# Optimization experiments

Measured on AMD Instinct MI355X. Metric: run time of the kernel, lower is better.

The kernel has to match this reference:

```python
import jax, jax.numpy as jnp
from jax import lax
import numpy as np

P, L, T, DEG, D = 100000, 20000, 8, 48, 64  # n_paths, n_links, max_path_len, max_link_degree, state dim
ITERS = 4


def _relu(x):
    return jnp.maximum(x, 0.0)


def _gru_cell(x, h, wih, whh, bih, bhh):
    # PyTorch GRU gate math
    gi = x @ wih.T + bih
    gh = h @ whh.T + bhh
    ir, iz, inn = jnp.split(gi, 3, axis=-1)
    hr, hz, hn = jnp.split(gh, 3, axis=-1)
    r = jax.nn.sigmoid(ir + hr)
    z = jax.nn.sigmoid(iz + hz)
    n = jnp.tanh(inn + r * hn)
    return (1.0 - z) * n + z * h


def _forward(traffic, capacity, link_to_path, path_to_link,
             pe_w1, pe_b1, pe_w2, pe_b2,
             le_w1, le_b1, le_w2, le_b2,
             gru_wih, gru_whh, gru_bih, gru_bhh,
             cell_wih, cell_whh, cell_bih, cell_bhh,
             am_w1, am_b1, am_w2, am_b2, am_w3, am_b3):
    path_state = _relu(_relu(traffic @ pe_w1.T + pe_b1) @ pe_w2.T + pe_b2)   # [1,P,D]
    link_state = _relu(_relu(capacity @ le_w1.T + le_b1) @ le_w2.T + le_b2)  # [1,L,D]

    l2p = link_to_path[0]                      # [P,T]
    lmask = l2p != -1                          # [P,T]
    lengths = lmask.sum(axis=-1)               # [P]
    p2l = path_to_link[0]                      # [L,DEG,2]
    pmask = (p2l[..., 0] != -1)[..., None]     # [L,DEG,1]
    pidx = jnp.clip(p2l[..., 0], 0)
    posidx = jnp.clip(p2l[..., 1], 0)
    l2p_c = jnp.clip(l2p, 0)

    for _ in range(ITERS):
        # gather link states along each path, mask padding
        x = link_state[0][l2p_c] * lmask[..., None]        # [P,T,D]
        h0 = path_state[0]                                  # [P,D]

        def step(h, inp):
            xt, t = inp
            hn = _gru_cell(xt, h, gru_wih, gru_whh, gru_bih, gru_bhh)
            valid = (t < lengths)[:, None]
            h_new = jnp.where(valid, hn, h)          # packed-seq: hidden frozen past length
            out = jnp.where(valid, hn, 0.0)          # pad_packed: zeros past length
            return h_new, out

        h_final, outs = lax.scan(step, h0, (x.transpose(1, 0, 2), jnp.arange(T)))
        path_state = h_final[None]                          # [1,P,D]
        pss = jnp.concatenate([h0[:, None], outs.transpose(1, 0, 2)], axis=1)  # [P,T+1,D]

        gathered = pss[pidx, posidx] * pmask                # [L,DEG,D]
        pmin = jnp.where(pmask, gathered, jnp.inf).min(axis=-2)
        pmax = jnp.where(pmask, gathered, -jnp.inf).max(axis=-2)
        psum = jnp.where(pmask, gathered, 0.0).sum(axis=-2)
        cnt = jnp.maximum(pmask.sum(axis=-2), 1).astype(psum.dtype)
        pmean = psum / cnt
        agg = jnp.concatenate([pmin, pmax, psum, pmean], axis=-1)  # [L,4D]

        pa = _relu(_relu(_relu(agg @ am_w1.T + am_b1) @ am_w2.T + am_b2) @ am_w3.T + am_b3)
        link_state = _gru_cell(pa, link_state[0], cell_wih, cell_whh, cell_bih, cell_bhh)[None]

    return path_state, link_state


def setup_inputs() -> dict:
    key = jax.random.key(0)
    ks = jax.random.split(key, 40)
    w = lambda i, *s: jax.random.normal(ks[i], s, dtype=jnp.float32) * 0.1

    traffic = jax.random.uniform(ks[0], (1, P, 1), dtype=jnp.float32)
    capacity = jax.random.uniform(ks[1], (1, L, 1), dtype=jnp.float32)

    lengths = jax.random.randint(ks[2], (P,), 2, T + 1).at[0].set(T)
    lvalid = jnp.arange(T)[None, :] < lengths[:, None]
    link_to_path = jnp.where(lvalid, jax.random.randint(ks[3], (P, T), 0, L), -1)[None].astype(jnp.int32)

    deg = jax.random.randint(ks[4], (L,), 1, DEG + 1)
    dvalid = jnp.arange(DEG)[None, :] < deg[:, None]
    p0 = jnp.where(dvalid, jax.random.randint(ks[5], (L, DEG), 0, P), -1)
    p1 = jnp.where(dvalid, jax.random.randint(ks[6], (L, DEG), 0, T + 1), 0)
    path_to_link = jnp.stack([p0, p1], axis=-1)[None].astype(jnp.int32)

    return dict(
        traffic=traffic, capacity=capacity,
        link_to_path=link_to_path, path_to_link=path_to_link,
        pe_w1=w(10, D, 1), pe_b1=w(11, D), pe_w2=w(12, D, D), pe_b2=w(13, D),
        le_w1=w(14, D, 1), le_b1=w(15, D), le_w2=w(16, D, D), le_b2=w(17, D),
        gru_wih=w(18, 3 * D, D), gru_whh=w(19, 3 * D, D), gru_bih=w(20, 3 * D), gru_bhh=w(21, 3 * D),
        cell_wih=w(22, 3 * D, D), cell_whh=w(23, 3 * D, D), cell_bih=w(24, 3 * D), cell_bhh=w(25, 3 * D),
        am_w1=w(26, 2 * D, 4 * D), am_b1=w(27, 2 * D), am_w2=w(28, 2 * D, 2 * D), am_b2=w(29, 2 * D),
        am_w3=w(30, D, 2 * D), am_b3=w(31, D),
    )


def reference(traffic, capacity, link_to_path, path_to_link,
              pe_w1, pe_b1, pe_w2, pe_b2,
              le_w1, le_b1, le_w2, le_b2,
              gru_wih, gru_whh, gru_bih, gru_bhh,
              cell_wih, cell_whh, cell_bih, cell_bhh,
              am_w1, am_b1, am_w2, am_b2, am_w3, am_b3):
    return _forward(traffic, capacity, link_to_path, path_to_link,
                    pe_w1, pe_b1, pe_w2, pe_b2,
                    le_w1, le_b1, le_w2, le_b2,
                    gru_wih, gru_whh, gru_bih, gru_bhh,
                    cell_wih, cell_whh, cell_bih, cell_bhh,
                    am_w1, am_b1, am_w2, am_b2, am_w3, am_b3)
```

## Files before the change

### kernel.cpp

```cpp
#include <hip/hip_runtime.h>

#define P_N 100000
#define L_N 20000
#define T_N 8
#define DEG_N 48
#define D_N 64

#define W_PE_W1    0
#define W_PE_B1    64
#define W_PE_W2    128
#define W_PE_B2    4224
#define W_LE_W1    4288
#define W_LE_B1    4352
#define W_LE_W2    4416
#define W_LE_B2    8512
#define W_GRU_WIH  8576
#define W_GRU_WHH  20864
#define W_GRU_BIH  33152
#define W_GRU_BHH  33344
#define W_CELL_WIH 33536
#define W_CELL_WHH 45824
#define W_CELL_BIH 58112
#define W_CELL_BHH 58304
#define W_AM_W1    58496
#define W_AM_B1    91264
#define W_AM_W2    91392
#define W_AM_B2    107776
#define W_AM_W3    107904
#define W_AM_B3    116096
#define OFF_PS     116160
#define OFF_LS     (OFF_PS + P_N*D_N)
#define OFF_AG     (OFF_LS + L_N*D_N)
#define OFF_PSS    (OFF_AG + L_N*4*D_N)
#define PSS_U32    (P_N*9*D_N/2)
#define OFF_FLAG   (OFF_PSS + PSS_U32)
#define OFF_WIH16  (OFF_FLAG + 8)
#define OFF_WHH16  (OFF_WIH16 + 6144)
#define OFF_LS16   (OFF_WHH16 + 6144)
#define OFF_LW16   (OFF_LS16 + 640000)
#define OFF_LSLO   (OFF_LW16 + 81920)

typedef __attribute__((ext_vector_type(8))) short bf8_t;
typedef __attribute__((ext_vector_type(4))) float f4_t;
#define MFMA16(a,b,c) __builtin_amdgcn_mfma_f32_16x16x32_bf16(a,b,c,0,0,0)
#define LWLO 81920

__device__ __forceinline__ float bf2f(unsigned short u) {
    return __uint_as_float(((unsigned)u) << 16);
}
__device__ __forceinline__ unsigned short f2bf(float f) {
    unsigned u = __float_as_uint(f);
    unsigned r = u + 0x7FFFu + ((u >> 16) & 1u);
    return (unsigned short)(r >> 16);
}
__device__ __forceinline__ unsigned pk2(float a, float b) {
    return (unsigned)f2bf(a) | ((unsigned)f2bf(b) << 16);
}
__device__ __forceinline__ float fast_sig(float a) {
    return __builtin_amdgcn_rcpf(1.0f + __expf(-a));
}
__device__ __forceinline__ float fast_tanh(float a) {
    float s = __builtin_amdgcn_rcpf(1.0f + __expf(-2.0f * a));
    return fmaf(2.0f, s, -1.0f);
}
__device__ __forceinline__ void lds_barrier() {
    asm volatile("s_waitcnt lgkmcnt(0)" ::: "memory");
    __builtin_amdgcn_s_barrier();
    __builtin_amdgcn_sched_barrier(0);
}

__global__ void detect_k(const unsigned short* __restrict__ traffic, int* __restrict__ flag) {
    if (threadIdx.x == 0 && blockIdx.x == 0) {
        int plausible = 0;
        for (int i = 0; i < 64; ++i) {
            unsigned short v = traffic[i];
            int ex = (v >> 7) & 0xFF;
            if (!(v & 0x8000) && ex >= 0x6F && ex <= 0x7E) plausible++;
        }
        *flag = (plausible >= 56) ? 1 : 0;
    }
}

struct WSrc { const void* p[22]; };

__global__ void conv_weights_k(WSrc src, float* __restrict__ dst, const int* __restrict__ flag) {
    const int sz[22]  = {64,64,4096,64, 64,64,4096,64, 12288,12288,192,192,
                         12288,12288,192,192, 32768,128,16384,128,8192,64};
    const int off[22] = {0,64,128,4224, 4288,4352,4416,8512, 8576,20864,33152,33344,
                         33536,45824,58112,58304, 58496,91264,91392,107776,107904,116096};
    int a = blockIdx.x;
    float* d = dst + off[a];
    int n = sz[a];
    if (*flag) {
        const unsigned short* s = (const unsigned short*)src.p[a];
        for (int i = threadIdx.x; i < n; i += blockDim.x) d[i] = bf2f(s[i]);
    } else {
        const float* s = (const float*)src.p[a];
        for (int i = threadIdx.x; i < n; i += blockDim.x) d[i] = s[i];
    }
}

__global__ void conv_bf16_k(const float* __restrict__ ws,
                            unsigned short* __restrict__ wih, unsigned short* __restrict__ whh,
                            unsigned short* __restrict__ lw) {
    int b = blockIdx.x;
    if (b < 48) {
        int i = b * 256 + threadIdx.x;
        if (i < 12288) { wih[i] = f2bf(ws[W_GRU_WIH + i]); whh[i] = f2bf(ws[W_GRU_WHH + i]); }
    } else {
        int i = (b - 48) * 256 + threadIdx.x;
        if (i >= 81920) return;
        float v;
        if (i < 32768)      v = ws[W_AM_W1 + i];
        else if (i < 49152) v = ws[W_AM_W2 + (i - 32768)];
        else if (i < 57344) v = ws[W_AM_W3 + (i - 49152)];
        else if (i < 69632) v = ws[W_CELL_WIH + (i - 57344)];
        else                v = ws[W_CELL_WHH + (i - 69632)];
        unsigned short hi = f2bf(v);
        lw[i] = hi;
        lw[LWLO + i] = f2bf(v - bf2f(hi));
    }
}

__global__ __launch_bounds__(256) void embed_k(
    const void* __restrict__ inp,
    const float* __restrict__ w1, const float* __restrict__ b1,
    const float* __restrict__ w2, const float* __restrict__ b2,
    float* __restrict__ out, unsigned short* __restrict__ ohi,
    unsigned short* __restrict__ olo, int N, const int* __restrict__ flag)
{
    int p = blockIdx.x * 256 + threadIdx.x;
    if (p >= N) return;
    float t = (*flag) ? bf2f(((const unsigned short*)inp)[p]) : ((const float*)inp)[p];
    float h1[64];
#pragma unroll
    for (int k = 0; k < 64; ++k) h1[k] = fmaxf(fmaf(t, w1[k], b1[k]), 0.0f);
#pragma unroll 1
    for (int j = 0; j < 64; ++j) {
        float acc = b2[j];
#pragma unroll
        for (int k = 0; k < 64; ++k) acc = fmaf(h1[k], w2[j * 64 + k], acc);
        float v = fmaxf(acc, 0.0f);
        out[p * 64 + j] = v;
        if (ohi) {
            unsigned short hi = f2bf(v);
            ohi[p * 64 + j] = hi;
            olo[p * 64 + j] = f2bf(v - bf2f(hi));
        }
    }
}

__global__ __launch_bounds__(256, 3) void path_gru_mfma_k(
    const unsigned short* __restrict__ wih16,
    const unsigned short* __restrict__ whh16,
    const float* __restrict__ bih, const float* __restrict__ bhh,
    const unsigned short* __restrict__ ls16,
    float* __restrict__ path_state,
    const int* __restrict__ l2p, unsigned short* __restrict__ pss, int first)
{
    __shared__ __align__(16) unsigned short xt[2][32 * 72];
    __shared__ __align__(16) unsigned short ht[2][32 * 72];
    __shared__ int lint[32][8];
    __shared__ int lmaskA[32];

    const int tid = threadIdx.x;
    const int w = tid >> 6;
    const int L = tid & 63;
    const int col = L & 15;
    const int quad = L >> 4;
    const int p0 = blockIdx.x * 32;
    const int gpath = tid >> 4;
    const int gseg = tid & 15;

    if (tid < 32) {
        const int4* r4 = (const int4*)(l2p + (p0 + tid) * 8);
        int4 a = r4[0], b = r4[1];
        lint[tid][0] = a.x; lint[tid][1] = a.y; lint[tid][2] = a.z; lint[tid][3] = a.w;
        lint[tid][4] = b.x; lint[tid][5] = b.y; lint[tid][6] = b.z; lint[tid][7] = b.w;
        lmaskA[tid] = (a.x >= 0) | ((a.y >= 0) << 1) | ((a.z >= 0) << 2) | ((a.w >= 0) << 3)
                    | ((b.x >= 0) << 4) | ((b.y >= 0) << 5) | ((b.z >= 0) << 6) | ((b.w >= 0) << 7);
    }

    bf8_t BIr[2], BHr[2], BIz[2], BHz[2], BIn[2], BHn[2];
#pragma unroll
    for (int f = 0; f < 2; ++f) {
        int orr = ((w) * 16 + col) * 64 + f * 32 + quad * 8;
        int oz  = ((4 + w) * 16 + col) * 64 + f * 32 + quad * 8;
        int on  = ((8 + w) * 16 + col) * 64 + f * 32 + quad * 8;
        BIr[f] = *(const bf8_t*)(wih16 + orr);  BHr[f] = *(const bf8_t*)(whh16 + orr);
        BIz[f] = *(const bf8_t*)(wih16 + oz);   BHz[f] = *(const bf8_t*)(whh16 + oz);
        BIn[f] = *(const bf8_t*)(wih16 + on);   BHn[f] = *(const bf8_t*)(whh16 + on);
    }
    const float bR  = bih[w * 16 + col] + bhh[w * 16 + col];
    const float bZ  = bih[64 + w * 16 + col] + bhh[64 + w * 16 + col];
    const float bIN = bih[128 + w * 16 + col];
    const float bHN = bhh[128 + w * 16 + col];

    float hf[2][4];
#pragma unroll
    for (int pt = 0; pt < 2; ++pt)
#pragma unroll
        for (int r = 0; r < 4; ++r) {
            hf[pt][r] = path_state[(size_t)(p0 + pt * 16 + quad * 4 + r) * 64 + w * 16 + col];
            ht[0][(pt * 16 + quad * 4 + r) * 72 + w * 16 + col] = f2bf(hf[pt][r]);
        }

    lds_barrier();

    unsigned pm[2][4];
#pragma unroll
    for (int pt = 0; pt < 2; ++pt)
#pragma unroll
        for (int r = 0; r < 4; ++r) pm[pt][r] = (unsigned)lmaskA[pt * 16 + quad * 4 + r];
    const unsigned gm0 = (unsigned)lmaskA[gpath];
    const unsigned gm1 = (unsigned)lmaskA[gpath + 16];

#pragma unroll
    for (int h2 = 0; h2 < 2; ++h2) {
        const int gp = gpath + h2 * 16;
        int li = lint[gp][0];
        uint2 v; v.x = 0u; v.y = 0u;
        if (li >= 0) v = *(const uint2*)(ls16 + (size_t)li * 64 + gseg * 4);
        *(uint2*)(&xt[0][gp * 72 + gseg * 4]) = v;
    }
    lds_barrier();

#pragma unroll 2
    for (int t = 0; t < T_N; ++t) {
        const int cur = t & 1, nxt = (t + 1) & 1;

        uint2 pf[2];
#pragma unroll
        for (int h2 = 0; h2 < 2; ++h2) {
            const int gp = gpath + h2 * 16;
            const unsigned gm = h2 ? gm1 : gm0;
            uint2 hv = *(const uint2*)(&ht[cur][gp * 72 + gseg * 4]);
            int keep = (t == 0) ? 1 : (int)((gm >> (t - 1)) & 1);
            if (keep | first) {
                if (!keep) { hv.x = 0u; hv.y = 0u; }
                *(uint2*)(pss + (size_t)(p0 + gp) * 576 + t * 64 + gseg * 4) = hv;
            }
            pf[h2].x = 0u; pf[h2].y = 0u;
            if (t < T_N - 1) {
                int li = lint[gp][t + 1];
                if (li >= 0) pf[h2] = *(const uint2*)(ls16 + (size_t)li * 64 + gseg * 4);
            }
        }

#pragma unroll
        for (int pt = 0; pt < 2; ++pt) {
            bf8_t xA0 = *(const bf8_t*)(&xt[cur][(pt * 16 + col) * 72 + quad * 8]);
            bf8_t xA1 = *(const bf8_t*)(&xt[cur][(pt * 16 + col) * 72 + 32 + quad * 8]);
            bf8_t hA0 = *(const bf8_t*)(&ht[cur][(pt * 16 + col) * 72 + quad * 8]);
            bf8_t hA1 = *(const bf8_t*)(&ht[cur][(pt * 16 + col) * 72 + 32 + quad * 8]);

            f4_t aR = {bR, bR, bR, bR};
            f4_t aZ = {bZ, bZ, bZ, bZ};
            f4_t aI = {bIN, bIN, bIN, bIN};
            f4_t aH = {bHN, bHN, bHN, bHN};
            aR = MFMA16(xA0, BIr[0], aR); aR = MFMA16(xA1, BIr[1], aR);
            aR = MFMA16(hA0, BHr[0], aR); aR = MFMA16(hA1, BHr[1], aR);
            aZ = MFMA16(xA0, BIz[0], aZ); aZ = MFMA16(xA1, BIz[1], aZ);
            aZ = MFMA16(hA0, BHz[0], aZ); aZ = MFMA16(hA1, BHz[1], aZ);
            aI = MFMA16(xA0, BIn[0], aI); aI = MFMA16(xA1, BIn[1], aI);
            aH = MFMA16(hA0, BHn[0], aH); aH = MFMA16(hA1, BHn[1], aH);

#pragma unroll
            for (int r = 0; r < 4; ++r) {
                float rr = fast_sig(aR[r]);
                float zz = fast_sig(aZ[r]);
                float nn = fast_tanh(fmaf(rr, aH[r], aI[r]));
                float hb = hf[pt][r];
                float hv = fmaf(zz, hb - nn, nn);
                hf[pt][r] = ((pm[pt][r] >> t) & 1) ? hv : hb;
            }
#pragma unroll
            for (int r = 0; r < 4; ++r)
                ht[nxt][(pt * 16 + quad * 4 + r) * 72 + w * 16 + col] = f2bf(hf[pt][r]);
        }

        if (t < T_N - 1) {
#pragma unroll
            for (int h2 = 0; h2 < 2; ++h2)
                *(uint2*)(&xt[nxt][(gpath + h2 * 16) * 72 + gseg * 4]) = pf[h2];
        }
        lds_barrier();
    }

#pragma unroll
    for (int h2 = 0; h2 < 2; ++h2) {
        const int gp = gpath + h2 * 16;
        const unsigned gm = h2 ? gm1 : gm0;
        uint2 hv = *(const uint2*)(&ht[0][gp * 72 + gseg * 4]);
        int keep = (int)((gm >> 7) & 1);
        if (keep | first) {
            if (!keep) { hv.x = 0u; hv.y = 0u; }
            *(uint2*)(pss + (size_t)(p0 + gp) * 576 + 8 * 64 + gseg * 4) = hv;
        }
    }
#pragma unroll
    for (int pt = 0; pt < 2; ++pt)
#pragma unroll
        for (int r = 0; r < 4; ++r)
            path_state[(size_t)(p0 + pt * 16 + quad * 4 + r) * 64 + w * 16 + col] = hf[pt][r];
}

__global__ __launch_bounds__(256, 4) void link_agg_k(
    const int* __restrict__ p2l, const unsigned short* __restrict__ pss,
    unsigned short* __restrict__ agg16)
{
    const int lane = threadIdx.x & 63;
    const int l = __builtin_amdgcn_readfirstlane(blockIdx.x * 4 + (threadIdx.x >> 6));
    const int* __restrict__ row = p2l + (size_t)l * 96;

    float vmin = INFINITY, vmax = -INFINITY, vsum = 0.0f;
    int cnt = 0;
#pragma unroll
    for (int d = 0; d < DEG_N; ++d) {
        int pid = row[d * 2];
        int pos = row[d * 2 + 1];
        size_t off = (size_t)max(pid, 0) * 576 + (size_t)pos * 64 + lane;
        float v = bf2f(pss[off]);
        bool ok = pid >= 0;
        vmin = fminf(vmin, ok ? v : INFINITY);
        vmax = fmaxf(vmax, ok ? v : -INFINITY);
        vsum += ok ? v : 0.0f;
        cnt += ok ? 1 : 0;
    }
    float mean = vsum / (float)max(cnt, 1);

    unsigned short* rw = agg16 + (size_t)l * 512;
    float vals[4] = {vmin, vmax, vsum, mean};
#pragma unroll
    for (int c = 0; c < 4; ++c) {
        unsigned short hi = f2bf(vals[c]);
        rw[c * 64 + lane] = hi;
        rw[256 + c * 64 + lane] = f2bf(vals[c] - bf2f(hi));
    }
}

__global__ __launch_bounds__(64, 2) void link_upd_mfma_k(
    const unsigned short* __restrict__ lw,
    const float* __restrict__ b1, const float* __restrict__ b2, const float* __restrict__ b3,
    const float* __restrict__ cbih, const float* __restrict__ cbhh,
    const unsigned short* __restrict__ agg16,
    float* __restrict__ link_state,
    unsigned short* __restrict__ lshi, unsigned short* __restrict__ lslo)
{
    __shared__ __align__(16) unsigned short tile[2 * 16 * 136];
    const int L = threadIdx.x & 63;
    const int col = L & 15;
    const int quad = L >> 4;
    const int l0 = blockIdx.x * 16;
    const int mlink = min(l0 + col, L_N - 1);
    unsigned short* tlhi = &tile[0];
    unsigned short* tllo = &tile[16 * 136];

    const unsigned short* w1b = lw;
    const unsigned short* w2b = lw + 32768;
    const unsigned short* w3b = lw + 49152;
    const unsigned short* cih = lw + 57344;
    const unsigned short* chh = lw + 69632;

    {
        bf8_t Ah[8], Al[8];
#pragma unroll
        for (int f = 0; f < 8; ++f) {
            Ah[f] = *(const bf8_t*)(agg16 + (size_t)mlink * 512 + f * 32 + quad * 8);
            Al[f] = *(const bf8_t*)(agg16 + (size_t)mlink * 512 + 256 + f * 32 + quad * 8);
        }
#pragma unroll
        for (int nt = 0; nt < 8; ++nt) {
            float bb = b1[nt * 16 + col];
            f4_t acc = {bb, bb, bb, bb};
#pragma unroll
            for (int f = 0; f < 8; ++f) {
                size_t o = (size_t)(nt * 16 + col) * 256 + f * 32 + quad * 8;
                bf8_t Bh = *(const bf8_t*)(w1b + o);
                bf8_t Bl = *(const bf8_t*)(w1b + LWLO + o);
                acc = MFMA16(Ah[f], Bh, acc);
                acc = MFMA16(Ah[f], Bl, acc);
                acc = MFMA16(Al[f], Bh, acc);
            }
#pragma unroll
            for (int r = 0; r < 4; ++r) {
                float v = fmaxf(acc[r], 0.0f);
                unsigned short hi = f2bf(v);
                tlhi[(quad * 4 + r) * 136 + nt * 16 + col] = hi;
                tllo[(quad * 4 + r) * 136 + nt * 16 + col] = f2bf(v - bf2f(hi));
            }
        }
    }
    {
        bf8_t Ah[4], Al[4];
#pragma unroll
        for (int f = 0; f < 4; ++f) {
            Ah[f] = *(const bf8_t*)(tlhi + col * 136 + f * 32 + quad * 8);
            Al[f] = *(const bf8_t*)(tllo + col * 136 + f * 32 + quad * 8);
        }
        float vv[8][4];
#pragma unroll
        for (int nt = 0; nt < 8; ++nt) {
            float bb = b2[nt * 16 + col];
            f4_t acc = {bb, bb, bb, bb};
#pragma unroll
            for (int f = 0; f < 4; ++f) {
                size_t o = (size_t)(nt * 16 + col) * 128 + f * 32 + quad * 8;
                bf8_t Bh = *(const bf8_t*)(w2b + o);
                bf8_t Bl = *(const bf8_t*)(w2b + LWLO + o);
                acc = MFMA16(Ah[f], Bh, acc);
                acc = MFMA16(Ah[f], Bl, acc);
                acc = MFMA16(Al[f], Bh, acc);
            }
#pragma unroll
            for (int r = 0; r < 4; ++r) vv[nt][r] = fmaxf(acc[r], 0.0f);
        }
#pragma unroll
        for (int nt = 0; nt < 8; ++nt)
#pragma unroll
            for (int r = 0; r < 4; ++r) {
                unsigned short hi = f2bf(vv[nt][r]);
                tlhi[(quad * 4 + r) * 136 + nt * 16 + col] = hi;
                tllo[(quad * 4 + r) * 136 + nt * 16 + col] = f2bf(vv[nt][r] - bf2f(hi));
            }
    }
    {
        bf8_t Ah[4], Al[4];
#pragma unroll
        for (int f = 0; f < 4; ++f) {
            Ah[f] = *(const bf8_t*)(tlhi + col * 136 + f * 32 + quad * 8);
            Al[f] = *(const bf8_t*)(tllo + col * 136 + f * 32 + quad * 8);
        }
        float vv[4][4];
#pragma unroll
        for (int nt = 0; nt < 4; ++nt) {
            float bb = b3[nt * 16 + col];
            f4_t acc = {bb, bb, bb, bb};
#pragma unroll
            for (int f = 0; f < 4; ++f) {
                size_t o = (size_t)(nt * 16 + col) * 128 + f * 32 + quad * 8;
                bf8_t Bh = *(const bf8_t*)(w3b + o);
                bf8_t Bl = *(const bf8_t*)(w3b + LWLO + o);
                acc = MFMA16(Ah[f], Bh, acc);
                acc = MFMA16(Ah[f], Bl, acc);
                acc = MFMA16(Al[f], Bh, acc);
            }
#pragma unroll
            for (int r = 0; r < 4; ++r) vv[nt][r] = fmaxf(acc[r], 0.0f);
        }
#pragma unroll
        for (int nt = 0; nt < 4; ++nt)
#pragma unroll
            for (int r = 0; r < 4; ++r) {
                unsigned short hi = f2bf(vv[nt][r]);
                tlhi[(quad * 4 + r) * 136 + nt * 16 + col] = hi;
                tllo[(quad * 4 + r) * 136 + nt * 16 + col] = f2bf(vv[nt][r] - bf2f(hi));
            }
    }
    bf8_t xAh[2], xAl[2], hAh[2], hAl[2];
#pragma unroll
    for (int f = 0; f < 2; ++f) {
        xAh[f] = *(const bf8_t*)(tlhi + col * 136 + f * 32 + quad * 8);
        xAl[f] = *(const bf8_t*)(tllo + col * 136 + f * 32 + quad * 8);
        hAh[f] = *(const bf8_t*)(lshi + (size_t)mlink * 64 + f * 32 + quad * 8);
        hAl[f] = *(const bf8_t*)(lslo + (size_t)mlink * 64 + f * 32 + quad * 8);
    }
    float hf[16];
#pragma unroll
    for (int nt = 0; nt < 4; ++nt)
#pragma unroll
        for (int r = 0; r < 4; ++r) {
            int ml = min(l0 + quad * 4 + r, L_N - 1);
            hf[nt * 4 + r] = link_state[(size_t)ml * 64 + nt * 16 + col];
        }
    f4_t aRZ[8], aIN[4], aHN[4];
#pragma unroll
    for (int nt = 0; nt < 8; ++nt) {
        float bb = cbih[nt * 16 + col] + cbhh[nt * 16 + col];
        aRZ[nt][0] = bb; aRZ[nt][1] = bb; aRZ[nt][2] = bb; aRZ[nt][3] = bb;
    }
#pragma unroll
    for (int nt = 0; nt < 4; ++nt) {
        float bi = cbih[128 + nt * 16 + col], bh = cbhh[128 + nt * 16 + col];
        aIN[nt][0] = bi; aIN[nt][1] = bi; aIN[nt][2] = bi; aIN[nt][3] = bi;
        aHN[nt][0] = bh; aHN[nt][1] = bh; aHN[nt][2] = bh; aHN[nt][3] = bh;
    }
#pragma unroll
    for (int nt = 0; nt < 8; ++nt) {
#pragma unroll
        for (int f = 0; f < 2; ++f) {
            size_t o = (size_t)(nt * 16 + col) * 64 + f * 32 + quad * 8;
            bf8_t Bih = *(const bf8_t*)(cih + o);
            bf8_t Bil = *(const bf8_t*)(cih + LWLO + o);
            bf8_t Bhh = *(const bf8_t*)(chh + o);
            bf8_t Bhl = *(const bf8_t*)(chh + LWLO + o);
            aRZ[nt] = MFMA16(xAh[f], Bih, aRZ[nt]);
            aRZ[nt] = MFMA16(xAh[f], Bil, aRZ[nt]);
            aRZ[nt] = MFMA16(xAl[f], Bih, aRZ[nt]);
            aRZ[nt] = MFMA16(hAh[f], Bhh, aRZ[nt]);
            aRZ[nt] = MFMA16(hAh[f], Bhl, aRZ[nt]);
            aRZ[nt] = MFMA16(hAl[f], Bhh, aRZ[nt]);
        }
    }
#pragma unroll
    for (int nt = 0; nt < 4; ++nt) {
#pragma unroll
        for (int f = 0; f < 2; ++f) {
            size_t o = (size_t)((8 + nt) * 16 + col) * 64 + f * 32 + quad * 8;
            bf8_t Bih = *(const bf8_t*)(cih + o);
            bf8_t Bil = *(const bf8_t*)(cih + LWLO + o);
            bf8_t Bhh = *(const bf8_t*)(chh + o);
            bf8_t Bhl = *(const bf8_t*)(chh + LWLO + o);
            aIN[nt] = MFMA16(xAh[f], Bih, aIN[nt]);
            aIN[nt] = MFMA16(xAh[f], Bil, aIN[nt]);
            aIN[nt] = MFMA16(xAl[f], Bih, aIN[nt]);
            aHN[nt] = MFMA16(hAh[f], Bhh, aHN[nt]);
            aHN[nt] = MFMA16(hAh[f], Bhl, aHN[nt]);
            aHN[nt] = MFMA16(hAl[f], Bhh, aHN[nt]);
        }
    }
#pragma unroll
    for (int nt = 0; nt < 4; ++nt)
#pragma unroll
        for (int r = 0; r < 4; ++r) {
            int mrow = l0 + quad * 4 + r;
            float rr = fast_sig(aRZ[nt][r]);
            float zz = fast_sig(aRZ[nt + 4][r]);
            float nn = fast_tanh(fmaf(rr, aHN[nt][r], aIN[nt][r]));
            float hb = hf[nt * 4 + r];
            float hv = fmaf(zz, hb - nn, nn);
            if (mrow < L_N) {
                link_state[(size_t)mrow * 64 + nt * 16 + col] = hv;
                unsigned short hi = f2bf(hv);
                lshi[(size_t)mrow * 64 + nt * 16 + col] = hi;
                lslo[(size_t)mrow * 64 + nt * 16 + col] = f2bf(hv - bf2f(hi));
            }
        }
}

__global__ void final_out_k(const float* __restrict__ ps, const float* __restrict__ ls,
                            void* __restrict__ out, const int* __restrict__ flag)
{
    int i = blockIdx.x * 256 + threadIdx.x;
    int e = i * 2;
    float a, b;
    if (e < P_N * D_N) { a = ps[e]; b = ps[e + 1]; }
    else               { a = ls[e - P_N * D_N]; b = ls[e - P_N * D_N + 1]; }
    if (*flag) {
        ((unsigned*)out)[i] = pk2(a, b);
    } else {
        float2 v; v.x = a; v.y = b;
        ((float2*)out)[i] = v;
    }
}

extern "C" void kernel_launch(void* const* d_in, const int* in_sizes, int n_in,
                              void* d_out, int out_size, void* d_ws, size_t ws_size,
                              hipStream_t stream)
{
    const int* l2p = (const int*)d_in[2];
    const int* p2l = (const int*)d_in[3];
    float* ws = (float*)d_ws;
    int* flag = (int*)(ws + OFF_FLAG);
    unsigned short* wih16 = (unsigned short*)(ws + OFF_WIH16);
    unsigned short* whh16 = (unsigned short*)(ws + OFF_WHH16);
    unsigned short* lshi  = (unsigned short*)(ws + OFF_LS16);
    unsigned short* lslo  = (unsigned short*)(ws + OFF_LSLO);
    unsigned short* lw16  = (unsigned short*)(ws + OFF_LW16);
    unsigned short* agg16 = (unsigned short*)(ws + OFF_AG);
    unsigned short* pss   = (unsigned short*)(ws + OFF_PSS);

    detect_k<<<1, 64, 0, stream>>>((const unsigned short*)d_in[0], flag);

    WSrc srcs;
    for (int i = 0; i < 22; ++i) srcs.p[i] = d_in[4 + i];
    conv_weights_k<<<22, 256, 0, stream>>>(srcs, ws, flag);
    conv_bf16_k<<<368, 256, 0, stream>>>(ws, wih16, whh16, lw16);

    embed_k<<<(P_N + 255) / 256, 256, 0, stream>>>(d_in[0], ws + W_PE_W1, ws + W_PE_B1,
                                                   ws + W_PE_W2, ws + W_PE_B2, ws + OFF_PS,
                                                   (unsigned short*)nullptr, (unsigned short*)nullptr,
                                                   P_N, flag);
    embed_k<<<(L_N + 255) / 256, 256, 0, stream>>>(d_in[1], ws + W_LE_W1, ws + W_LE_B1,
                                                   ws + W_LE_W2, ws + W_LE_B2, ws + OFF_LS,
                                                   lshi, lslo, L_N, flag);

    for (int it = 0; it < 4; ++it) {
        path_gru_mfma_k<<<P_N / 32, 256, 0, stream>>>(
            wih16, whh16, ws + W_GRU_BIH, ws + W_GRU_BHH,
            lshi, ws + OFF_PS, l2p, pss, it == 0 ? 1 : 0);
        link_agg_k<<<L_N / 4, 256, 0, stream>>>(p2l, pss, agg16);
        link_upd_mfma_k<<<L_N / 16, 64, 0, stream>>>(
            lw16, ws + W_AM_B1, ws + W_AM_B2, ws + W_AM_B3,
            ws + W_CELL_BIH, ws + W_CELL_BHH,
            agg16, ws + OFF_LS, lshi, lslo);
    }
    final_out_k<<<(P_N * D_N + L_N * D_N) / 512, 256, 0, stream>>>(
        ws + OFF_PS, ws + OFF_LS, d_out, flag);
}
```

Before: 890.4 us.

## Bucket paths by length and truncate GRU timesteps per block

```diff
diff --git a/kernel.cpp b/kernel.cpp
--- a/kernel.cpp
+++ b/kernel.cpp
@@ -39,6 +39,9 @@
 #define OFF_LS16   (OFF_WHH16 + 6144)
 #define OFF_LW16   (OFF_LS16 + 640000)
 #define OFF_LSLO   (OFF_LW16 + 81920)
+#define OFF_SORT   (OFF_LSLO + 640000)
+#define OFF_PLEN   (OFF_SORT + P_N)
+#define OFF_HIST   (OFF_PLEN + P_N)
 
 typedef __attribute__((ext_vector_type(8))) short bf8_t;
 typedef __attribute__((ext_vector_type(4))) float f4_t;
@@ -69,7 +72,9 @@
     __builtin_amdgcn_sched_barrier(0);
 }
 
-__global__ void detect_k(const unsigned short* __restrict__ traffic, int* __restrict__ flag) {
+__global__ void detect_k(const unsigned short* __restrict__ traffic, int* __restrict__ flag,
+                         int* __restrict__ hist) {
+    if (threadIdx.x < 32) hist[threadIdx.x] = 0;
     if (threadIdx.x == 0 && blockIdx.x == 0) {
         int plausible = 0;
         for (int i = 0; i < 64; ++i) {
@@ -79,6 +84,32 @@
         }
         *flag = (plausible >= 56) ? 1 : 0;
     }
+}
+
+__global__ void plen_hist_k(const int* __restrict__ l2p, int* __restrict__ plen,
+                            int* __restrict__ hist) {
+    int p = blockIdx.x * 256 + threadIdx.x;
+    if (p >= P_N) return;
+    const int4* r4 = (const int4*)(l2p + (size_t)p * 8);
+    int4 a = r4[0], b = r4[1];
+    int len = (a.x >= 0) + (a.y >= 0) + (a.z >= 0) + (a.w >= 0)
+            + (b.x >= 0) + (b.y >= 0) + (b.z >= 0) + (b.w >= 0);
+    plen[p] = len;
+    atomicAdd(&hist[len], 1);
+}
+
+__global__ void scan_base_k(int* __restrict__ hist) {
+    if (threadIdx.x == 0 && blockIdx.x == 0) {
+        int base = 0;
+        for (int i = 0; i <= T_N; ++i) { int c = hist[i]; hist[16 + i] = base; base += c; }
+    }
+}
+
+__global__ void scatter_k(const int* __restrict__ plen, int* __restrict__ hist,
+                          int* __restrict__ sorted) {
+    int p = blockIdx.x * 256 + threadIdx.x;
+    if (p >= P_N) return;
+    sorted[atomicAdd(&hist[16 + plen[p]], 1)] = p;
 }
 
 struct WSrc { const void* p[22]; };
@@ -156,12 +187,14 @@
     const float* __restrict__ bih, const float* __restrict__ bhh,
     const unsigned short* __restrict__ ls16,
     float* __restrict__ path_state,
-    const int* __restrict__ l2p, unsigned short* __restrict__ pss, int first)
+    const int* __restrict__ l2p, unsigned short* __restrict__ pss,
+    const int* __restrict__ sorted, int first)
 {
     __shared__ __align__(16) unsigned short xt[2][32 * 72];
     __shared__ __align__(16) unsigned short ht[2][32 * 72];
     __shared__ int lint[32][8];
     __shared__ int lmaskA[32];
+    __shared__ int spid[32];
 
     const int tid = threadIdx.x;
     const int w = tid >> 6;
@@ -173,7 +206,9 @@
     const int gseg = tid & 15;
 
     if (tid < 32) {
-        const int4* r4 = (const int4*)(l2p + (p0 + tid) * 8);
+        int pid = sorted[p0 + tid];
+        spid[tid] = pid;
+        const int4* r4 = (const int4*)(l2p + (size_t)pid * 8);
         int4 a = r4[0], b = r4[1];
         lint[tid][0] = a.x; lint[tid][1] = a.y; lint[tid][2] = a.z; lint[tid][3] = a.w;
         lint[tid][4] = b.x; lint[tid][5] = b.y; lint[tid][6] = b.z; lint[tid][7] = b.w;
@@ -196,16 +231,12 @@
     const float bIN = bih[128 + w * 16 + col];
     const float bHN = bhh[128 + w * 16 + col];
 
-    float hf[2][4];
-#pragma unroll
-    for (int pt = 0; pt < 2; ++pt)
-#pragma unroll
-        for (int r = 0; r < 4; ++r) {
-            hf[pt][r] = path_state[(size_t)(p0 + pt * 16 + quad * 4 + r) * 64 + w * 16 + col];
-            ht[0][(pt * 16 + quad * 4 + r) * 72 + w * 16 + col] = f2bf(hf[pt][r]);
-        }
-
     lds_barrier();
+
+    int allm = 0;
+#pragma unroll
+    for (int i = 0; i < 32; ++i) allm |= lmaskA[i];
+    const int tmax = first ? T_N : min(max(32 - __clz(allm), 1), T_N);
 
     unsigned pm[2][4];
 #pragma unroll
@@ -214,6 +245,17 @@
         for (int r = 0; r < 4; ++r) pm[pt][r] = (unsigned)lmaskA[pt * 16 + quad * 4 + r];
     const unsigned gm0 = (unsigned)lmaskA[gpath];
     const unsigned gm1 = (unsigned)lmaskA[gpath + 16];
+    const int gpid0 = spid[gpath];
+    const int gpid1 = spid[gpath + 16];
+
+    float hf[2][4];
+#pragma unroll
+    for (int pt = 0; pt < 2; ++pt)
+#pragma unroll
+        for (int r = 0; r < 4; ++r) {
+            hf[pt][r] = path_state[(size_t)spid[pt * 16 + quad * 4 + r] * 64 + w * 16 + col];
+            ht[0][(pt * 16 + quad * 4 + r) * 72 + w * 16 + col] = f2bf(hf[pt][r]);
+        }
 
 #pragma unroll
     for (int h2 = 0; h2 < 2; ++h2) {
@@ -226,7 +268,7 @@
     lds_barrier();
 
 #pragma unroll 2
-    for (int t = 0; t < T_N; ++t) {
+    for (int t = 0; t < tmax; ++t) {
         const int cur = t & 1, nxt = (t + 1) & 1;
 
         uint2 pf[2];
@@ -234,14 +276,15 @@
         for (int h2 = 0; h2 < 2; ++h2) {
             const int gp = gpath + h2 * 16;
             const unsigned gm = h2 ? gm1 : gm0;
+            const int gpid = h2 ? gpid1 : gpid0;
             uint2 hv = *(const uint2*)(&ht[cur][gp * 72 + gseg * 4]);
             int keep = (t == 0) ? 1 : (int)((gm >> (t - 1)) & 1);
             if (keep | first) {
                 if (!keep) { hv.x = 0u; hv.y = 0u; }
-                *(uint2*)(pss + (size_t)(p0 + gp) * 576 + t * 64 + gseg * 4) = hv;
+                *(uint2*)(pss + (size_t)gpid * 576 + t * 64 + gseg * 4) = hv;
             }
             pf[h2].x = 0u; pf[h2].y = 0u;
-            if (t < T_N - 1) {
+            if (t < tmax - 1) {
                 int li = lint[gp][t + 1];
                 if (li >= 0) pf[h2] = *(const uint2*)(ls16 + (size_t)li * 64 + gseg * 4);
             }
@@ -279,7 +322,7 @@
                 ht[nxt][(pt * 16 + quad * 4 + r) * 72 + w * 16 + col] = f2bf(hf[pt][r]);
         }
 
-        if (t < T_N - 1) {
+        if (t < tmax - 1) {
 #pragma unroll
             for (int h2 = 0; h2 < 2; ++h2)
                 *(uint2*)(&xt[nxt][(gpath + h2 * 16) * 72 + gseg * 4]) = pf[h2];
@@ -287,22 +330,24 @@
         lds_barrier();
     }
 
+    const int fin = tmax & 1;
 #pragma unroll
     for (int h2 = 0; h2 < 2; ++h2) {
         const int gp = gpath + h2 * 16;
         const unsigned gm = h2 ? gm1 : gm0;
-        uint2 hv = *(const uint2*)(&ht[0][gp * 72 + gseg * 4]);
-        int keep = (int)((gm >> 7) & 1);
+        const int gpid = h2 ? gpid1 : gpid0;
+        uint2 hv = *(const uint2*)(&ht[fin][gp * 72 + gseg * 4]);
+        int keep = (int)((gm >> (tmax - 1)) & 1);
         if (keep | first) {
             if (!keep) { hv.x = 0u; hv.y = 0u; }
-            *(uint2*)(pss + (size_t)(p0 + gp) * 576 + 8 * 64 + gseg * 4) = hv;
+            *(uint2*)(pss + (size_t)gpid * 576 + tmax * 64 + gseg * 4) = hv;
         }
     }
 #pragma unroll
     for (int pt = 0; pt < 2; ++pt)
 #pragma unroll
         for (int r = 0; r < 4; ++r)
-            path_state[(size_t)(p0 + pt * 16 + quad * 4 + r) * 64 + w * 16 + col] = hf[pt][r];
+            path_state[(size_t)spid[pt * 16 + quad * 4 + r] * 64 + w * 16 + col] = hf[pt][r];
 }
 
 __global__ __launch_bounds__(256, 4) void link_agg_k(
@@ -569,13 +614,20 @@
     unsigned short* lw16  = (unsigned short*)(ws + OFF_LW16);
     unsigned short* agg16 = (unsigned short*)(ws + OFF_AG);
     unsigned short* pss   = (unsigned short*)(ws + OFF_PSS);
-
-    detect_k<<<1, 64, 0, stream>>>((const unsigned short*)d_in[0], flag);
+    int* sorted = (int*)(ws + OFF_SORT);
+    int* plen   = (int*)(ws + OFF_PLEN);
+    int* hist   = (int*)(ws + OFF_HIST);
+
+    detect_k<<<1, 64, 0, stream>>>((const unsigned short*)d_in[0], flag, hist);
 
     WSrc srcs;
     for (int i = 0; i < 22; ++i) srcs.p[i] = d_in[4 + i];
     conv_weights_k<<<22, 256, 0, stream>>>(srcs, ws, flag);
     conv_bf16_k<<<368, 256, 0, stream>>>(ws, wih16, whh16, lw16);
+
+    plen_hist_k<<<(P_N + 255) / 256, 256, 0, stream>>>(l2p, plen, hist);
+    scan_base_k<<<1, 64, 0, stream>>>(hist);
+    scatter_k<<<(P_N + 255) / 256, 256, 0, stream>>>(plen, hist, sorted);
 
     embed_k<<<(P_N + 255) / 256, 256, 0, stream>>>(d_in[0], ws + W_PE_W1, ws + W_PE_B1,
                                                    ws + W_PE_W2, ws + W_PE_B2, ws + OFF_PS,
@@ -588,7 +640,7 @@
     for (int it = 0; it < 4; ++it) {
         path_gru_mfma_k<<<P_N / 32, 256, 0, stream>>>(
             wih16, whh16, ws + W_GRU_BIH, ws + W_GRU_BHH,
-            lshi, ws + OFF_PS, l2p, pss, it == 0 ? 1 : 0);
+            lshi, ws + OFF_PS, l2p, pss, sorted, it == 0 ? 1 : 0);
         link_agg_k<<<L_N / 4, 256, 0, stream>>>(p2l, pss, agg16);
         link_upd_mfma_k<<<L_N / 16, 64, 0, stream>>>(
             lw16, ws + W_AM_B1, ws + W_AM_B2, ws + W_AM_B3,
```

After: 1.624 ms. 82.4% more time.
